# Performance work log

Measured on AMD Instinct MI355X. Metric: run time of the kernel, lower is better.

The kernel has to match this reference:

```python
import jax, jax.numpy as jnp
import numpy as np

H, KVH, HD = 32, 8, 128          # query heads, kv heads, head_dim
HIDDEN = H * HD                   # 4096
TOTAL_KV = 3072                   # sum of (start_pos + seqlen) over the batch (static)
ROPE_THETA = 10000.0


def setup_inputs() -> dict:
    key = jax.random.key(0)
    ks = jax.random.split(key, 4)
    x = jax.random.normal(ks[0], (1024, HIDDEN), jnp.float32)
    wqkv = jax.random.normal(ks[1], (HIDDEN, HIDDEN + 2 * KVH * HD), jnp.float32) * 0.02
    wo = jax.random.normal(ks[2], (HIDDEN, HIDDEN), jnp.float32) * 0.02
    # paged cache: [num_layers=1, 2(k/v), cache_slots, kv_heads, head_dim], holds post-RoPE prefixes
    kv_cache = jax.random.normal(ks[3], (1, 2, 8192, KVH, HD), jnp.float32) * 0.02
    # 4 ragged requests: seqlens [512,256,128,128], cached prefixes [0,512,1024,512]
    seqstarts = jnp.array([0, 512, 768, 896, 1024], jnp.int32)
    start_pos = jnp.array([0, 512, 1024, 512], jnp.int32)
    kvstarts = jnp.array([0, 512, 1280, 2432, 3072], jnp.int32)  # cumsum of start_pos+seqlen
    cachestarts = jnp.array([0, 1024, 2560, 4096], jnp.int32)    # page base per request
    return dict(x=x, wqkv=wqkv, wo=wo, kv_cache=kv_cache, seqstarts=seqstarts,
                kvstarts=kvstarts, cachestarts=cachestarts, start_pos=start_pos)


def _rope(t, pos):
    # interleaved (GPT-J style) rotary over full head_dim; t: [T, nheads, HD], pos: [T]
    d2 = HD // 2
    inv_freq = 1.0 / (ROPE_THETA ** (jnp.arange(d2, dtype=jnp.float32) / d2))
    ang = pos.astype(jnp.float32)[:, None] * inv_freq      # [T, d2]
    cos = jnp.cos(ang)[:, None, :]
    sin = jnp.sin(ang)[:, None, :]
    x1, x2 = t[..., 0::2], t[..., 1::2]
    r1 = x1 * cos - x2 * sin
    r2 = x1 * sin + x2 * cos
    return jnp.stack([r1, r2], axis=-1).reshape(t.shape)


def _forward(x, wqkv, wo, kv_cache, seqstarts, kvstarts, cachestarts, start_pos):
    T = x.shape[0]
    # fused QKV projection
    xqkv = (x @ wqkv).reshape(T, H + 2 * KVH, HD)
    xq, xk, xv = jnp.split(xqkv, [H, H + KVH], axis=1)   # [T,32,HD],[T,8,HD],[T,8,HD]

    # per-token batch id and absolute position (ragged via seqstarts)
    tok = jnp.arange(T)
    bq = jnp.searchsorted(seqstarts, tok, side='right') - 1
    pos_q = tok - seqstarts[bq] + start_pos[bq]
    xq = _rope(xq, pos_q)
    xk = _rope(xk, pos_q)

    # assemble ragged KV stream: cached prefix (paged cache) + freshly projected tokens
    kvtok = jnp.arange(TOTAL_KV)
    bkv = jnp.searchsorted(kvstarts, kvtok, side='right') - 1
    pkv = kvtok - kvstarts[bkv]                              # absolute kv position
    is_new = pkv >= start_pos[bkv]
    new_idx = jnp.clip(seqstarts[bkv] + pkv - start_pos[bkv], 0, T - 1)
    cache_idx = cachestarts[bkv] + pkv                       # paged slot for prefix
    keys = jnp.where(is_new[:, None, None], xk[new_idx], kv_cache[0, 0][cache_idx])
    vals = jnp.where(is_new[:, None, None], xv[new_idx], kv_cache[0, 1][cache_idx])

    # GQA: repeat kv heads to match query heads
    rep = H // KVH
    keys = jnp.repeat(keys, rep, axis=1)                     # [TOTAL_KV, 32, HD]
    vals = jnp.repeat(vals, rep, axis=1)

    scale = 1.0 / jnp.sqrt(jnp.float32(HD))
    scores = jnp.einsum('qhd,khd->hqk', xq, keys) * scale    # [32, T, TOTAL_KV]
    # ragged causal mask: same request and kv position <= query position
    mask = (bq[:, None] == bkv[None, :]) & (pkv[None, :] <= pos_q[:, None])
    scores = jnp.where(mask[None], scores, jnp.float32(-1e30))
    probs = jax.nn.softmax(scores, axis=-1)
    attn = jnp.einsum('hqk,khd->qhd', probs, vals)           # [T, 32, HD]
    return attn.reshape(T, HIDDEN) @ wo


def reference(x, wqkv, wo, kv_cache, seqstarts, kvstarts, cachestarts, start_pos):
    return _forward(x, wqkv, wo, kv_cache, seqstarts, kvstarts, cachestarts, start_pos)
```

## Files before the change

kernel.cpp:

```cpp
#include <hip/hip_runtime.h>
#include <hip/hip_bf16.h>
#include <math.h>
#include <stdint.h>

typedef __bf16 bf16;
typedef __attribute__((ext_vector_type(4))) float floatx4;
typedef __attribute__((ext_vector_type(8))) bf16 bf16x8;
typedef __attribute__((ext_vector_type(4))) bf16 bf16x4;

#define LDS_ASYNC16(gptr, lptr)                                                \
  __builtin_amdgcn_global_load_lds(                                            \
      (const __attribute__((address_space(1))) void*)(gptr),                   \
      (__attribute__((address_space(3))) void*)(lptr), 16, 0, 0)

__global__ __launch_bounds__(256) void k_cvt(const float* __restrict__ in,
                                             bf16* __restrict__ out) {
  int i = (blockIdx.x * 256 + threadIdx.x) * 4;
  float4 v = *(const float4*)(in + i);
  bf16x4 o;
  o[0] = (bf16)v.x; o[1] = (bf16)v.y; o[2] = (bf16)v.z; o[3] = (bf16)v.w;
  *(bf16x4*)(out + i) = o;
}

__global__ __launch_bounds__(256) void k_merge(const float* __restrict__ a,
                                               const float* __restrict__ b,
                                               float* __restrict__ out) {
  int i = (blockIdx.x * 256 + threadIdx.x) * 4;
  float4 va = *(const float4*)(a + i);
  float4 vb = *(const float4*)(b + i);
  float4 o;
  o.x = va.x + vb.x; o.y = va.y + vb.y; o.z = va.z + vb.z; o.w = va.w + vb.w;
  *(float4*)(out + i) = o;
}

__global__ __launch_bounds__(256) void k_transpose_cvt(const float* __restrict__ in,
                                                       bf16* __restrict__ out,
                                                       int K, int N) {
  __shared__ float tile[64][65];
  int k0 = blockIdx.y * 64, n0 = blockIdx.x * 64;
  int tid = threadIdx.x;
  int cg = tid & 15, rr = tid >> 4;
#pragma unroll
  for (int p = 0; p < 4; ++p) {
    int r = rr + p * 16;
    float4 v = *(const float4*)(in + (size_t)(k0 + r) * N + n0 + cg * 4);
    tile[r][cg * 4 + 0] = v.x; tile[r][cg * 4 + 1] = v.y;
    tile[r][cg * 4 + 2] = v.z; tile[r][cg * 4 + 3] = v.w;
  }
  __syncthreads();
#pragma unroll
  for (int p = 0; p < 4; ++p) {
    int n = rr + p * 16;
    bf16x4 o;
    o[0] = (bf16)tile[cg * 4 + 0][n];
    o[1] = (bf16)tile[cg * 4 + 1][n];
    o[2] = (bf16)tile[cg * 4 + 2][n];
    o[3] = (bf16)tile[cg * 4 + 3][n];
    *(bf16x4*)(out + (size_t)(n0 + n) * K + k0 + cg * 4) = o;
  }
}

__global__ __launch_bounds__(512) void k_gemm8(const bf16* __restrict__ A,
                                               const bf16* __restrict__ B,
                                               float* __restrict__ C,
                                               int M, int N, int K, int ksplit) {
  __shared__ bf16 As[3][128 * 64];
  __shared__ bf16 Bs[3][256 * 64];
  int tid = threadIdx.x;
  int w = tid >> 6, lane = tid & 63;
  int lq = lane >> 4, l16 = lane & 15;
  int wr = w >> 2, wc = w & 3;
  int bm = blockIdx.y * 128, bn = blockIdx.x * 256;
  int kc = K / ksplit;
  int NT = kc >> 6;
  C += (size_t)blockIdx.z * M * N;
  const bf16* Ab = A + (size_t)bm * K + blockIdx.z * kc;
  const bf16* Bb = B + (size_t)bn * K + blockIdx.z * kc;
  int srow = w * 8 + (lane >> 3);
  int sx = ((lane & 7) ^ (srow & 7)) * 8;
  const bf16* Asrc = Ab + (size_t)srow * K + sx;
  const bf16* Bsrc = Bb + (size_t)srow * K + sx;
  bf16* AL = &As[0][0] + w * 8 * 64;
  bf16* BL = &Bs[0][0] + w * 8 * 64;

#define STAGE8(bi, t)                                                          \
  do {                                                                         \
    const bf16* a_ = Asrc + (size_t)(t) * 64;                                  \
    const bf16* b_ = Bsrc + (size_t)(t) * 64;                                  \
    LDS_ASYNC16(a_, AL + (bi) * (128 * 64));                                   \
    LDS_ASYNC16(a_ + (size_t)64 * K, AL + (bi) * (128 * 64) + 64 * 64);        \
    LDS_ASYNC16(b_, BL + (bi) * (256 * 64));                                   \
    LDS_ASYNC16(b_ + (size_t)64 * K, BL + (bi) * (256 * 64) + 64 * 64);        \
    LDS_ASYNC16(b_ + (size_t)128 * K, BL + (bi) * (256 * 64) + 128 * 64);      \
    LDS_ASYNC16(b_ + (size_t)192 * K, BL + (bi) * (256 * 64) + 192 * 64);      \
  } while (0)

  STAGE8(0, 0);
  STAGE8(1, 1);

  int aoff[4][2], boff[4][2];
#pragma unroll
  for (int i = 0; i < 4; ++i)
#pragma unroll
    for (int kk = 0; kk < 2; ++kk) {
      int sw = ((kk * 4 + lq) ^ (l16 & 7)) * 8;
      aoff[i][kk] = (wr * 64 + i * 16 + l16) * 64 + sw;
      boff[i][kk] = (wc * 64 + i * 16 + l16) * 64 + sw;
    }

  floatx4 acc[4][4] = {};

  auto compute_tile = [&](int bcc) {
    const bf16* Ar = &As[bcc][0];
    const bf16* Br = &Bs[bcc][0];
    bf16x8 af[4][2], bg[4][2];
#pragma unroll
    for (int i = 0; i < 4; ++i)
#pragma unroll
      for (int kk = 0; kk < 2; ++kk) {
        af[i][kk] = *(const bf16x8*)(Ar + aoff[i][kk]);
        bg[i][kk] = *(const bf16x8*)(Br + boff[i][kk]);
      }
    __builtin_amdgcn_s_setprio(1);
#pragma unroll
    for (int i = 0; i < 4; ++i)
#pragma unroll
      for (int j = 0; j < 4; ++j)
#pragma unroll
        for (int kk = 0; kk < 2; ++kk)
          acc[i][j] = __builtin_amdgcn_mfma_f32_16x16x32_bf16(af[i][kk], bg[j][kk],
                                                              acc[i][j], 0, 0, 0);
    __builtin_amdgcn_s_setprio(0);
  };

  int bc = 0;
  for (int t = 0; t < NT - 1; ++t) {
    asm volatile("s_waitcnt vmcnt(6)" ::: "memory");
    __builtin_amdgcn_s_barrier();
    __builtin_amdgcn_sched_barrier(0);
    if (t + 2 < NT) {
      int bs = bc + 2; if (bs >= 3) bs -= 3;
      STAGE8(bs, t + 2);
    }
    compute_tile(bc);
    ++bc; if (bc == 3) bc = 0;
  }
  asm volatile("s_waitcnt vmcnt(0)" ::: "memory");
  __builtin_amdgcn_s_barrier();
  __builtin_amdgcn_sched_barrier(0);
  compute_tile(bc);
#undef STAGE8

#pragma unroll
  for (int i = 0; i < 4; ++i)
#pragma unroll
    for (int j = 0; j < 4; ++j) {
      int m = bm + wr * 64 + i * 16 + lq * 4;
      int n = bn + wc * 64 + j * 16 + l16;
      float* cp = C + (size_t)m * N + n;
#pragma unroll
      for (int r = 0; r < 4; ++r) cp[(size_t)r * N] = acc[i][j][r];
    }
}

__global__ __launch_bounds__(256) void k_rope(const float* __restrict__ xp,
                                              bf16* __restrict__ qb,
                                              bf16* __restrict__ kb,
                                              const int* __restrict__ seqstarts,
                                              const int* __restrict__ start_pos) {
  int t = blockIdx.x;
  int s = 0;
  for (int i = 1; i < 4; ++i) if (seqstarts[i] <= t) s = i;
  float pos = (float)(t - seqstarts[s] + start_pos[s]);
  for (int wk = threadIdx.x; wk < 40 * 64; wk += 256) {
    int hh = wk >> 6, j = wk & 63;
    size_t idx = ((size_t)t * 48 + hh) * 128 + 2 * j;
    float2 a0 = *(const float2*)(xp + idx);
    float x1 = a0.x;
    float x2 = a0.y;
    float invf = exp2f(-(float)j * 0.20762050593045935f);
    float ang = pos * invf;
    float sv, cv;
    sincosf(ang, &sv, &cv);
    float r1 = x1 * cv - x2 * sv;
    float r2 = x1 * sv + x2 * cv;
    unsigned int u1 = (unsigned int)__builtin_bit_cast(unsigned short, (bf16)r1);
    unsigned int u2 = (unsigned int)__builtin_bit_cast(unsigned short, (bf16)r2);
    unsigned int pk = u1 | (u2 << 16);
    unsigned int* dst = (hh < 32)
        ? (unsigned int*)(qb + ((size_t)t * 32 + hh) * 128)
        : (unsigned int*)(kb + ((size_t)t * 8 + (hh - 32)) * 128);
    dst[j] = pk;
  }
}

__global__ __launch_bounds__(256) void k_assemble_k(
    const bf16* __restrict__ xk, const float* __restrict__ ck,
    bf16* __restrict__ kall,
    const int* __restrict__ seqstarts, const int* __restrict__ kvstarts,
    const int* __restrict__ cachestarts, const int* __restrict__ start_pos) {
  int p = blockIdx.x;
  int b = 0;
  for (int i = 1; i < 4; ++i) if (kvstarts[i] <= p) b = i;
  int pkv = p - kvstarts[b];
  int tid = threadIdx.x;
  int hk = tid >> 5, d4 = (tid & 31) * 4;
  bf16* dst = kall + ((size_t)hk * 3072 + p) * 128 + d4;
  if (pkv >= start_pos[b]) {
    int tn = seqstarts[b] + pkv - start_pos[b];
    *(bf16x4*)dst = *(const bf16x4*)(xk + ((size_t)tn * 8 + hk) * 128 + d4);
  } else {
    int ci = cachestarts[b] + pkv;
    float4 v = *(const float4*)(ck + ((size_t)ci * 8 + hk) * 128 + d4);
    bf16x4 o;
    o[0] = (bf16)v.x; o[1] = (bf16)v.y; o[2] = (bf16)v.z; o[3] = (bf16)v.w;
    *(bf16x4*)dst = o;
  }
}

__global__ __launch_bounds__(256) void k_assemble_vT(
    const float* __restrict__ xp,
    const float* __restrict__ cv, bf16* __restrict__ vT,
    const int* __restrict__ seqstarts, const int* __restrict__ kvstarts,
    const int* __restrict__ cachestarts, const int* __restrict__ start_pos) {
  __shared__ float tile[64][130];
  int hk = blockIdx.y, p0 = blockIdx.x * 64;
  int tid = threadIdx.x;
  {
    int r = tid >> 2;
    int p = p0 + r;
    int b = 0;
    for (int i = 1; i < 4; ++i) if (kvstarts[i] <= p) b = i;
    int pkv = p - kvstarts[b];
    int f0 = (tid & 3) * 32;
    if (pkv >= start_pos[b]) {
      int tn = seqstarts[b] + pkv - start_pos[b];
      size_t base = (size_t)tn * 6144 + (40 + hk) * 128;
#pragma unroll
      for (int i = 0; i < 8; ++i) {
        float4 v0 = *(const float4*)(xp + base + f0 + i * 4);
        tile[r][f0 + i * 4 + 0] = v0.x;
        tile[r][f0 + i * 4 + 1] = v0.y;
        tile[r][f0 + i * 4 + 2] = v0.z;
        tile[r][f0 + i * 4 + 3] = v0.w;
      }
    } else {
      int ci = cachestarts[b] + pkv;
      const float* src = cv + ((size_t)ci * 8 + hk) * 128;
#pragma unroll
      for (int i = 0; i < 8; ++i) {
        float4 v = *(const float4*)(src + f0 + i * 4);
        tile[r][f0 + i * 4 + 0] = v.x; tile[r][f0 + i * 4 + 1] = v.y;
        tile[r][f0 + i * 4 + 2] = v.z; tile[r][f0 + i * 4 + 3] = v.w;
      }
    }
  }
  __syncthreads();
  int d = tid >> 1, hf = tid & 1;
  bf16* dst = vT + ((size_t)hk * 128 + d) * 3072 + p0 + hf * 32;
#pragma unroll
  for (int q = 0; q < 4; ++q) {
    bf16x8 o;
#pragma unroll
    for (int e = 0; e < 8; ++e) o[e] = (bf16)tile[hf * 32 + q * 8 + e][d];
    *(bf16x8*)(dst + q * 8) = o;
  }
}

__global__ __launch_bounds__(256) void k_attn(
    const bf16* __restrict__ qb, const bf16* __restrict__ kall,
    const bf16* __restrict__ vT, float* __restrict__ pO,
    float2* __restrict__ pml,
    const int* __restrict__ seqstarts, const int* __restrict__ kvstarts,
    const int* __restrict__ start_pos) {
  __shared__ bf16 Ks[64 * 128];
  __shared__ bf16 Vs[128 * 64];
  __shared__ bf16 Ps[64 * 64];
  int qbi = blockIdx.x, h = blockIdx.y, seg = blockIdx.z, hk = h >> 2;
  int t0 = qbi * 64;
  int s = 0;
  for (int i = 1; i < 4; ++i) if (seqstarts[i] <= t0) s = i;
  int posbase = t0 - seqstarts[s] + start_pos[s];
  int kv0 = kvstarts[s];
  int nkv = posbase + 64;
  int pbeg = seg * 512;
  if (pbeg >= nkv) return;
  int pend = min(pbeg + 512, nkv);
  int tid = threadIdx.x, w = tid >> 6, lane = tid & 63;
  int lq = lane >> 4, l16 = lane & 15;

  bf16x8 qa[4];
#pragma unroll
  for (int kk = 0; kk < 4; ++kk)
    qa[kk] = *(const bf16x8*)(qb + (((size_t)(t0 + w * 16 + l16) * 32 + h) * 128 +
                                    kk * 32 + lq * 8));

  int krow = lane >> 4;
  int vrow = lane >> 3;
  int vchunk = ((lane & 7) ^ (vrow & 7));
  int sw8 = l16 & 7;

  float m_r[4], l_r[4];
  floatx4 oacc[8] = {};
#pragma unroll
  for (int rg = 0; rg < 4; ++rg) { m_r[rg] = -3.0e38f; l_r[rg] = 0.f; }
  const float scale = 0.08838834764831845f;

  for (int p0 = pbeg; p0 < pend; p0 += 64) {
#pragma unroll
    for (int c = 0; c < 4; ++c) {
      int base_r = w * 16 + c * 4;
      int r = base_r + krow;
      int gch = (lane & 15) ^ ((c * 4 + krow) & 15);
      LDS_ASYNC16(kall + (((size_t)hk * 3072 + kv0 + p0 + r) * 128 + gch * 8),
                  &Ks[base_r * 128]);
    }
#pragma unroll
    for (int c = 0; c < 4; ++c) {
      int base_d = w * 32 + c * 8;
      int d = base_d + vrow;
      LDS_ASYNC16(vT + (((size_t)hk * 128 + d) * 3072 + kv0 + p0 + vchunk * 8),
                  &Vs[base_d * 64]);
    }
    __syncthreads();

    floatx4 sacc[4] = {};
#pragma unroll
    for (int kk = 0; kk < 4; ++kk)
#pragma unroll
      for (int j = 0; j < 4; ++j) {
        bf16x8 kb = *(const bf16x8*)&Ks[(j * 16 + l16) * 128 +
                                        ((kk * 4 + lq) ^ l16) * 8];
        sacc[j] = __builtin_amdgcn_mfma_f32_16x16x32_bf16(qa[kk], kb, sacc[j], 0, 0, 0);
      }

#pragma unroll
    for (int rg = 0; rg < 4; ++rg) {
      int qpos = posbase + w * 16 + lq * 4 + rg;
      float sv[4];
      float rmax = -3.0e38f;
#pragma unroll
      for (int j = 0; j < 4; ++j) {
        int pkv = p0 + j * 16 + l16;
        sv[j] = (pkv <= qpos) ? sacc[j][rg] * scale : -3.0e38f;
        rmax = fmaxf(rmax, sv[j]);
      }
#pragma unroll
      for (int off = 1; off < 16; off <<= 1)
        rmax = fmaxf(rmax, __shfl_xor(rmax, off, 64));
      float mnew = fmaxf(m_r[rg], rmax);
      float alpha = __expf(m_r[rg] - mnew);
      m_r[rg] = mnew;
      int prow = w * 16 + lq * 4 + rg;
      int pswz = (lq * 4 + rg) & 7;
      float psum = 0.f;
#pragma unroll
      for (int j = 0; j < 4; ++j) {
        float pv = __expf(sv[j] - mnew);
        psum += pv;
        int chunk = (j * 2 + (l16 >> 3)) ^ pswz;
        Ps[prow * 64 + chunk * 8 + (l16 & 7)] = (bf16)pv;
      }
#pragma unroll
      for (int off = 1; off < 16; off <<= 1) psum += __shfl_xor(psum, off, 64);
      l_r[rg] = l_r[rg] * alpha + psum;
#pragma unroll
      for (int nt = 0; nt < 8; ++nt) oacc[nt][rg] *= alpha;
    }

#pragma unroll
    for (int kk = 0; kk < 2; ++kk) {
      bf16x8 pa = *(const bf16x8*)&Ps[(w * 16 + l16) * 64 +
                                      ((kk * 4 + lq) ^ sw8) * 8];
#pragma unroll
      for (int nt = 0; nt < 8; ++nt) {
        bf16x8 vb = *(const bf16x8*)&Vs[(nt * 16 + l16) * 64 +
                                        ((kk * 4 + lq) ^ sw8) * 8];
        oacc[nt] = __builtin_amdgcn_mfma_f32_16x16x32_bf16(pa, vb, oacc[nt], 0, 0, 0);
      }
    }
    __syncthreads();
  }

  size_t obase = (((size_t)seg * 16 + qbi) * 32 + h) * 8192;
#pragma unroll
  for (int rg = 0; rg < 4; ++rg) {
    int row = w * 16 + lq * 4 + rg;
#pragma unroll
    for (int nt = 0; nt < 8; ++nt)
      pO[obase + (size_t)row * 128 + nt * 16 + l16] = oacc[nt][rg];
    if (l16 == 0)
      pml[(((size_t)seg * 16 + qbi) * 32 + h) * 64 + row] =
          make_float2(m_r[rg], l_r[rg]);
  }
}

__global__ __launch_bounds__(256) void k_attn_merge(
    const float* __restrict__ pO, const float2* __restrict__ pml,
    bf16* __restrict__ aout,
    const int* __restrict__ seqstarts, const int* __restrict__ start_pos) {
  int qbi = blockIdx.x, h = blockIdx.y;
  int t0 = qbi * 64;
  int s = 0;
  for (int i = 1; i < 4; ++i) if (seqstarts[i] <= t0) s = i;
  int nkv = t0 - seqstarts[s] + start_pos[s] + 64;
  int ns = (nkv + 511) >> 9;
  int tid = threadIdx.x;
  int row = tid >> 2, cg = (tid & 3) * 32;
  float2 ml[3];
  float w[3];
  float mstar = -3.0e38f;
  for (int si = 0; si < ns; ++si) {
    ml[si] = pml[(((size_t)si * 16 + qbi) * 32 + h) * 64 + row];
    mstar = fmaxf(mstar, ml[si].x);
  }
  float denom = 0.f;
  for (int si = 0; si < ns; ++si) {
    w[si] = __expf(ml[si].x - mstar);
    denom += w[si] * ml[si].y;
  }
  float inv = 1.0f / denom;
  bf16* dst = aout + (size_t)(t0 + row) * 4096 + h * 128 + cg;
#pragma unroll
  for (int c = 0; c < 32; c += 8) {
    float acc[8] = {};
    for (int si = 0; si < ns; ++si) {
      const float* src = pO + (((size_t)si * 16 + qbi) * 32 + h) * 8192 +
                         (size_t)row * 128 + cg + c;
      float4 v0 = *(const float4*)(src);
      float4 v1 = *(const float4*)(src + 4);
      acc[0] += w[si] * v0.x; acc[1] += w[si] * v0.y;
      acc[2] += w[si] * v0.z; acc[3] += w[si] * v0.w;
      acc[4] += w[si] * v1.x; acc[5] += w[si] * v1.y;
      acc[6] += w[si] * v1.z; acc[7] += w[si] * v1.w;
    }
    bf16x8 o;
#pragma unroll
    for (int e = 0; e < 8; ++e) o[e] = (bf16)(acc[e] * inv);
    *(bf16x8*)(dst + c) = o;
  }
}

extern "C" void kernel_launch(void* const* d_in, const int* in_sizes, int n_in,
                              void* d_out, int out_size, void* d_ws, size_t ws_size,
                              hipStream_t stream) {
  const float* x = (const float*)d_in[0];
  const float* wqkv = (const float*)d_in[1];
  const float* wo = (const float*)d_in[2];
  const float* kv = (const float*)d_in[3];
  const int* seqstarts = (const int*)d_in[4];
  const int* kvstarts = (const int*)d_in[5];
  const int* cachestarts = (const int*)d_in[6];
  const int* start_pos = (const int*)d_in[7];
  float* out = (float*)d_out;

  char* base = (char*)d_ws;
  size_t off = 0;
  auto carve = [&](size_t bytes) {
    void* r = base + off;
    off += (bytes + 255) & ~(size_t)255;
    return r;
  };
  bf16* x_bf    = (bf16*)carve(1024ull * 4096 * 2);
  bf16* wqkvT   = (bf16*)carve(6144ull * 4096 * 2);
  bf16* woT     = (bf16*)carve(4096ull * 4096 * 2);
  float* xqkv   = (float*)carve(2ull * 1024 * 6144 * 4);
  bf16* q_bf    = (bf16*)carve(1024ull * 32 * 128 * 2);
  bf16* xk_bf   = (bf16*)carve(1024ull * 8 * 128 * 2);
  bf16* k_all   = (bf16*)carve(8ull * 3072 * 128 * 2);
  bf16* vT_all  = (bf16*)carve(8ull * 128 * 3072 * 2);
  bf16* attn_bf = (bf16*)carve(1024ull * 4096 * 2);
  float2* pml   = (float2*)carve(3ull * 16 * 32 * 64 * 8);
  float* outp = (float*)wqkvT;
  float* pO = xqkv;

  const float* cache_v = kv + 8192ull * 8 * 128;

  k_cvt<<<4096, 256, 0, stream>>>(x, x_bf);
  k_transpose_cvt<<<dim3(96, 64), 256, 0, stream>>>(wqkv, wqkvT, 4096, 6144);
  k_transpose_cvt<<<dim3(64, 64), 256, 0, stream>>>(wo, woT, 4096, 4096);
  k_gemm8<<<dim3(24, 8, 1), 512, 0, stream>>>(x_bf, wqkvT, xqkv, 1024, 6144,
                                              4096, 1);
  k_rope<<<1024, 256, 0, stream>>>(xqkv, q_bf, xk_bf, seqstarts, start_pos);
  k_assemble_k<<<3072, 256, 0, stream>>>(xk_bf, kv, k_all, seqstarts, kvstarts,
                                         cachestarts, start_pos);
  k_assemble_vT<<<dim3(48, 8), 256, 0, stream>>>(xqkv, cache_v, vT_all,
                                                 seqstarts, kvstarts, cachestarts,
                                                 start_pos);
  k_attn<<<dim3(16, 32, 3), 256, 0, stream>>>(q_bf, k_all, vT_all, pO, pml,
                                              seqstarts, kvstarts, start_pos);
  k_attn_merge<<<dim3(16, 32), 256, 0, stream>>>(pO, pml, attn_bf, seqstarts,
                                                 start_pos);
  k_gemm8<<<dim3(16, 8, 2), 512, 0, stream>>>(attn_bf, woT, outp, 1024, 4096,
                                              4096, 2);
  k_merge<<<4096, 256, 0, stream>>>(outp, outp + 1024ull * 4096, out);
}
```

Baseline: 488.4 us.

## Split GEMM main loop into four phases interleaving LDS reads, async loads, MFMA

Restructures the bf16 GEMM main loop into four quadrant phases. Each phase issues a subset of LDS fragment reads and a pair of async global-to-LDS loads, then runs a 2x2 quadrant of MFMAs, with barriers between phases. The aim is to spread memory traffic across the compute instead of issuing all loads up front, in the style of ping-pong scheduling. In exchange it adds several more block-wide barriers per K tile, and the vmcnt accounting is more complex.

Result: no change. 496.7 us (+1.7%).

```diff
diff --git a/kernel.cpp b/kernel.cpp
--- a/kernel.cpp
+++ b/kernel.cpp
@@ -83,20 +83,22 @@
   bf16* AL = &As[0][0] + w * 8 * 64;
   bf16* BL = &Bs[0][0] + w * 8 * 64;
 
-#define STAGE8(bi, t)                                                          \
-  do {                                                                         \
-    const bf16* a_ = Asrc + (size_t)(t) * 64;                                  \
-    const bf16* b_ = Bsrc + (size_t)(t) * 64;                                  \
-    LDS_ASYNC16(a_, AL + (bi) * (128 * 64));                                   \
-    LDS_ASYNC16(a_ + (size_t)64 * K, AL + (bi) * (128 * 64) + 64 * 64);        \
-    LDS_ASYNC16(b_, BL + (bi) * (256 * 64));                                   \
-    LDS_ASYNC16(b_ + (size_t)64 * K, BL + (bi) * (256 * 64) + 64 * 64);        \
-    LDS_ASYNC16(b_ + (size_t)128 * K, BL + (bi) * (256 * 64) + 128 * 64);      \
-    LDS_ASYNC16(b_ + (size_t)192 * K, BL + (bi) * (256 * 64) + 192 * 64);      \
-  } while (0)
-
-  STAGE8(0, 0);
-  STAGE8(1, 1);
+#define STAGE_PAIR(p0_, l0_, p1_, l1_)                                         \
+  do { LDS_ASYNC16(p0_, l0_); LDS_ASYNC16(p1_, l1_); } while (0)
+
+#pragma unroll
+  for (int pt = 0; pt < 2; ++pt) {
+    const bf16* a_ = Asrc + (size_t)pt * 64;
+    const bf16* b_ = Bsrc + (size_t)pt * 64;
+    bf16* ALs = AL + pt * (128 * 64);
+    bf16* BLs = BL + pt * (256 * 64);
+    LDS_ASYNC16(a_, ALs);
+    LDS_ASYNC16(a_ + (size_t)64 * K, ALs + 64 * 64);
+    LDS_ASYNC16(b_, BLs);
+    LDS_ASYNC16(b_ + (size_t)64 * K, BLs + 64 * 64);
+    LDS_ASYNC16(b_ + (size_t)128 * K, BLs + 128 * 64);
+    LDS_ASYNC16(b_ + (size_t)192 * K, BLs + 192 * 64);
+  }
 
   int aoff[4][2], boff[4][2];
 #pragma unroll
@@ -109,47 +111,81 @@
     }
 
   floatx4 acc[4][4] = {};
-
-  auto compute_tile = [&](int bcc) {
-    const bf16* Ar = &As[bcc][0];
-    const bf16* Br = &Bs[bcc][0];
-    bf16x8 af[4][2], bg[4][2];
-#pragma unroll
-    for (int i = 0; i < 4; ++i)
-#pragma unroll
-      for (int kk = 0; kk < 2; ++kk) {
-        af[i][kk] = *(const bf16x8*)(Ar + aoff[i][kk]);
-        bg[i][kk] = *(const bf16x8*)(Br + boff[i][kk]);
-      }
-    __builtin_amdgcn_s_setprio(1);
-#pragma unroll
-    for (int i = 0; i < 4; ++i)
-#pragma unroll
-      for (int j = 0; j < 4; ++j)
-#pragma unroll
-        for (int kk = 0; kk < 2; ++kk)
-          acc[i][j] = __builtin_amdgcn_mfma_f32_16x16x32_bf16(af[i][kk], bg[j][kk],
-                                                              acc[i][j], 0, 0, 0);
-    __builtin_amdgcn_s_setprio(0);
-  };
+  bf16x8 af[4][2], bg[4][2];
+
+#define LDA2(i_) do {                                                          \
+    af[i_][0] = *(const bf16x8*)(Ar + aoff[i_][0]);                            \
+    af[i_][1] = *(const bf16x8*)(Ar + aoff[i_][1]); } while (0)
+#define LDB2(j_) do {                                                          \
+    bg[j_][0] = *(const bf16x8*)(Br + boff[j_][0]);                            \
+    bg[j_][1] = *(const bf16x8*)(Br + boff[j_][1]); } while (0)
+#define MFMA_Q(i0_, j0_)                                                       \
+  do {                                                                         \
+    __builtin_amdgcn_s_setprio(1);                                             \
+    _Pragma("unroll")                                                          \
+    for (int i = (i0_); i < (i0_) + 2; ++i)                                    \
+      _Pragma("unroll")                                                        \
+      for (int j = (j0_); j < (j0_) + 2; ++j)                                  \
+        _Pragma("unroll")                                                      \
+        for (int kk = 0; kk < 2; ++kk)                                         \
+          acc[i][j] = __builtin_amdgcn_mfma_f32_16x16x32_bf16(                 \
+              af[i][kk], bg[j][kk], acc[i][j], 0, 0, 0);                       \
+    __builtin_amdgcn_s_setprio(0);                                             \
+  } while (0)
+#define PHASE_SYNC()                                                           \
+  do {                                                                         \
+    __builtin_amdgcn_s_barrier();                                              \
+    asm volatile("s_waitcnt lgkmcnt(0)" ::: "memory");                         \
+    __builtin_amdgcn_sched_barrier(0);                                         \
+  } while (0)
+
+  asm volatile("s_waitcnt vmcnt(6)" ::: "memory");
+  __builtin_amdgcn_s_barrier();
 
   int bc = 0;
-  for (int t = 0; t < NT - 1; ++t) {
-    asm volatile("s_waitcnt vmcnt(6)" ::: "memory");
+  for (int t = 0; t < NT; ++t) {
+    const bf16* Ar = &As[bc][0];
+    const bf16* Br = &Bs[bc][0];
+    int bs = bc + 2; if (bs >= 3) bs -= 3;
+    bool st = (t + 2 < NT);
+    const bf16* a_ = Asrc + (size_t)(t + 2) * 64;
+    const bf16* b_ = Bsrc + (size_t)(t + 2) * 64;
+    bf16* ALs = AL + bs * (128 * 64);
+    bf16* BLs = BL + bs * (256 * 64);
+
+    LDA2(0); LDA2(1); LDB2(0); LDB2(1);
+    if (st) STAGE_PAIR(a_, ALs, a_ + (size_t)64 * K, ALs + 64 * 64);
+    PHASE_SYNC();
+    MFMA_Q(0, 0);
     __builtin_amdgcn_s_barrier();
-    __builtin_amdgcn_sched_barrier(0);
-    if (t + 2 < NT) {
-      int bs = bc + 2; if (bs >= 3) bs -= 3;
-      STAGE8(bs, t + 2);
-    }
-    compute_tile(bc);
+
+    LDB2(2); LDB2(3);
+    if (st) STAGE_PAIR(b_, BLs, b_ + (size_t)64 * K, BLs + 64 * 64);
+    PHASE_SYNC();
+    MFMA_Q(0, 2);
+    __builtin_amdgcn_s_barrier();
+
+    LDA2(2); LDA2(3);
+    if (st) STAGE_PAIR(b_ + (size_t)128 * K, BLs + 128 * 64,
+                       b_ + (size_t)192 * K, BLs + 192 * 64);
+    PHASE_SYNC();
+    MFMA_Q(2, 0);
+    __builtin_amdgcn_s_barrier();
+
+    MFMA_Q(2, 2);
+    if (t + 2 < NT)
+      asm volatile("s_waitcnt vmcnt(6)" ::: "memory");
+    else if (t + 1 < NT)
+      asm volatile("s_waitcnt vmcnt(0)" ::: "memory");
+    __builtin_amdgcn_s_barrier();
+
     ++bc; if (bc == 3) bc = 0;
   }
-  asm volatile("s_waitcnt vmcnt(0)" ::: "memory");
-  __builtin_amdgcn_s_barrier();
-  __builtin_amdgcn_sched_barrier(0);
-  compute_tile(bc);
-#undef STAGE8
+#undef STAGE_PAIR
+#undef LDA2
+#undef LDB2
+#undef MFMA_Q
+#undef PHASE_SYNC
 
 #pragma unroll
   for (int i = 0; i < 4; ++i)
```
